# Optimization experiments

Hardware: AMD Instinct MI355X
Metric: run time of the kernel (lower is better)

Reference implementation:

```python
import jax, jax.numpy as jnp
import numpy as np

NEG = -1e30  # finite stand-in for -inf (keeps grads NaN-free)

def _rnnt_costs(log_probs, labels, lengths, label_lengths):
    """RNN-T negative log-likelihood per example.
    log_probs: (N, T, U, V) log-probabilities; labels: (N, U-1) int32;
    lengths, label_lengths: (N,) int32. blank = V-1 (module default).
    alpha recurrence: alpha[t,u] = LSE(alpha[t-1,u]+blank[t-1,u], alpha[t,u-1]+emit[t,u-1]).
    Each row-in-u linear log-recurrence is solved in parallel with cumlogsumexp:
    alpha[t,u] = c[u] + LSE_{k<=u}(A[k] - c[k]),  c = exclusive cumsum of emit[t], A = alpha[t-1]+blank[t-1].
    """
    N, T, U, V = log_probs.shape
    blank = V - 1
    blank_lp = log_probs[..., blank]  # (N, T, U)
    lbl = jnp.broadcast_to(labels[:, None, :, None], (N, T, U - 1, 1))
    emit = jnp.take_along_axis(log_probs[:, :, : U - 1, :], lbl, axis=3)[..., 0]  # (N, T, U-1)

    def row(A, emit_row):
        # A: (N, U) = alpha[t-1] + blank[t-1]; emit_row: (N, U-1) = emit[t]
        c = jnp.concatenate([jnp.zeros((N, 1), log_probs.dtype),
                             jnp.cumsum(emit_row, axis=1)], axis=1)  # (N, U)
        return c + jax.lax.cumlogsumexp(A - c, axis=1)

    A0 = jnp.full((N, U), NEG, log_probs.dtype).at[:, 0].set(0.0)
    alpha0 = row(A0, emit[:, 0, :])  # row t = 0

    def step(alpha_prev, xs):
        blank_prev, emit_row = xs  # (N, U), (N, U-1)
        alpha = row(alpha_prev + blank_prev, emit_row)
        return alpha, alpha

    xs = (jnp.swapaxes(blank_lp[:, :-1, :], 0, 1),  # (T-1, N, U)
          jnp.swapaxes(emit[:, 1:, :], 0, 1))       # (T-1, N, U-1)
    _, alphas = jax.lax.scan(step, alpha0, xs)
    alphas = jnp.concatenate([alpha0[None], alphas], axis=0)  # (T, N, U)

    n = jnp.arange(N)
    t_idx = lengths.astype(jnp.int32) - 1
    u_idx = label_lengths.astype(jnp.int32)
    loglik = alphas[t_idx, n, u_idx] + blank_lp[n, t_idx, u_idx]
    return -loglik  # (N,)


def setup_inputs() -> dict:
    key = jax.random.key(0)
    k1, k2, k3, k4 = jax.random.split(key, 4)
    N, T, U, V = 16, 256, 128, 256
    logits = jax.random.normal(k1, (N, T, U, V), dtype=jnp.float32)
    log_probs = jax.nn.log_softmax(logits, axis=-1)
    labels = jax.random.randint(k2, (N, U - 1), 0, V - 1, dtype=jnp.int32)  # never blank
    lengths = jax.random.randint(k3, (N,), T // 2, T + 1, dtype=jnp.int32).at[0].set(T)
    label_lengths = jax.random.randint(k4, (N,), (U - 1) // 2, U, dtype=jnp.int32).at[0].set(U - 1)
    return {"log_probs": log_probs, "labels": labels,
            "lengths": lengths, "label_lengths": label_lengths}


def reference(log_probs, labels, lengths, label_lengths):
    costs = _rnnt_costs(log_probs, labels, lengths, label_lengths)
    return jnp.mean(costs)  # reduction='mean'
```

## Files before the change

kernel.cpp:

```cpp
#include <hip/hip_runtime.h>


#define T_DIM 256
#define U_DIM 128
#define V_DIM 256
#define UV (U_DIM * V_DIM)
#define GROWS (T_DIM + 1)
#define NEGF (-1e30f)
#define LOG2E 1.44269504088896340736f
#define LN2F  0.69314718055994530942f

__device__ __forceinline__ float lse2b2(float x, float y) {
    float m = fmaxf(x, y);
    float t = __builtin_amdgcn_exp2f(-fabsf(x - y));
    return m + __builtin_amdgcn_logf(1.0f + t);
}

__device__ __forceinline__ float wave_shr1(float x) {
    int xi = __float_as_int(x);
    int r = __builtin_amdgcn_update_dpp(xi, xi, 0x138, 0xF, 0xF, false);
    return __int_as_float(r);
}

__global__ __launch_bounds__(128) void rnnt_gather_kernel(
        const float* __restrict__ lp, const int* __restrict__ labels,
        float2* __restrict__ G) {
    const int t = blockIdx.x;
    const int n = blockIdx.y;
    const int u = threadIdx.x;

    float x = NEGF, y = NEGF;
    if (t >= 1) {
        x = lp[((size_t)(n * T_DIM + (t - 1)) * U_DIM + u) * V_DIM + (V_DIM - 1)]
            * LOG2E;
    }
    if (u >= 1 && t < T_DIM) {
        const int lbl = labels[n * (U_DIM - 1) + (u - 1)];
        y = lp[((size_t)(n * T_DIM + t) * U_DIM + (u - 1)) * V_DIM + lbl] * LOG2E;
    }
    G[(size_t)n * GROWS * U_DIM + t * U_DIM + u] = make_float2(x, y);
}

__global__ __launch_bounds__(64, 1) void rnnt_diag_kernel(
        const float* __restrict__ lp, const float2* __restrict__ G,
        const int* __restrict__ lengths, const int* __restrict__ lab_lens,
        float* __restrict__ out, float inv_n) {
    const int n    = blockIdx.x;
    const int lane = threadIdx.x;
    const int u0   = lane * 2;
    const int u1   = u0 + 1;

    const float2* Gn = G + (size_t)n * GROWS * U_DIM;
    const float2* g0 = Gn + u0;
    const float2* g1 = Gn + u1;

    const int t_len = lengths[n];
    const int u_len = lab_lens[n];
    const int dstar = (t_len - 1) + u_len;

    const float bl = lp[(size_t)n * T_DIM * UV + (size_t)(t_len - 1) * UV
                        + u_len * V_DIM + (V_DIM - 1)];

    float a0 = (lane == 0) ? 0.0f : NEGF;
    float a1 = NEGF;
    float res = NEGF;
    if (dstar == 0 && lane == 0) res = a0;

    float nb = wave_shr1(a1);

    constexpr int PF = 16;
    float2 bufG0[PF], bufG1[PF];

    auto issue = [&](int d, int slot) {
        const int t0 = min(max(d - u0, 0), GROWS - 1);
        const int t1 = min(max(d - u1, 0), GROWS - 1);
        bufG0[slot] = g0[t0 * U_DIM];
        bufG1[slot] = g1[t1 * U_DIM];
    };

#pragma unroll
    for (int j = 0; j < PF; ++j) issue(1 + j, j);

    for (int dd = 1; dd < 385; dd += PF) {
#pragma unroll
        for (int j = 0; j < PF; ++j) {
            const int d = dd + j;
            const int t0 = d - u0;
            const int t1 = d - u1;
            const bool vb0 = (unsigned)(t0 - 1) < (unsigned)(T_DIM - 1);
            const bool vb1 = (unsigned)(t1 - 1) < (unsigned)(T_DIM - 1);
            const bool ve0 = (u0 >= 1) && ((unsigned)t0 < (unsigned)T_DIM);
            const bool ve1 = ((unsigned)t1 < (unsigned)T_DIM);

            const float pa0 = vb0 ? (a0 + bufG0[j].x) : NEGF;
            const float pb0 = ve0 ? (nb + bufG0[j].y) : NEGF;
            const float na0 = lse2b2(pa0, pb0);

            const float pa1 = vb1 ? (a1 + bufG1[j].x) : NEGF;
            const float pb1 = ve1 ? (a0 + bufG1[j].y) : NEGF;
            const float na1 = lse2b2(pa1, pb1);

            a0 = na0;
            a1 = na1;
            nb = wave_shr1(a1);

            issue(d + PF, j);

            if (d == dstar) {
                if (u_len == u0)      res = na0;
                else if (u_len == u1) res = na1;
            }
        }
    }

    if (lane == (u_len >> 1)) {
        atomicAdd(out, -(res * LN2F + bl) * inv_n);
    }
}

extern "C" void kernel_launch(void* const* d_in, const int* in_sizes, int n_in,
                              void* d_out, int out_size, void* d_ws, size_t ws_size,
                              hipStream_t stream) {
    const float* lp      = (const float*)d_in[0];
    const int*   labels  = (const int*)d_in[1];
    const int*   lengths = (const int*)d_in[2];
    const int*   lablens = (const int*)d_in[3];
    float* out = (float*)d_out;
    const int N = in_sizes[2];

    float2* G = (float2*)d_ws;

    hipMemsetAsync(d_out, 0, sizeof(float), stream);
    rnnt_gather_kernel<<<dim3(GROWS, N), dim3(128), 0, stream>>>(lp, labels, G);
    rnnt_diag_kernel<<<dim3(N), dim3(64), 0, stream>>>(
        lp, G, lengths, lablens, out, 1.0f / (float)N);
}
```

Before: 657.5 us.

## Relayout gathered blank/emit values into anti-diagonal order for coalesced loads

```diff
diff --git a/kernel.cpp b/kernel.cpp
--- a/kernel.cpp
+++ b/kernel.cpp
@@ -6,6 +6,7 @@
 #define V_DIM 256
 #define UV (U_DIM * V_DIM)
 #define GROWS (T_DIM + 1)
+#define E_ROWS 384
 #define NEGF (-1e30f)
 #define LOG2E 1.44269504088896340736f
 #define LN2F  0.69314718055994530942f
@@ -41,8 +42,20 @@
     G[(size_t)n * GROWS * U_DIM + t * U_DIM + u] = make_float2(x, y);
 }
 
+__global__ __launch_bounds__(128) void rnnt_relayout_kernel(
+        const float2* __restrict__ G, float2* __restrict__ Gd) {
+    const int e = blockIdx.x;
+    const int n = blockIdx.y;
+    const int u = threadIdx.x;
+    const int t = e - u;
+    float2 v = make_float2(NEGF, NEGF);
+    if ((unsigned)t <= (unsigned)T_DIM)
+        v = G[(size_t)n * GROWS * U_DIM + t * U_DIM + u];
+    Gd[(size_t)n * E_ROWS * U_DIM + e * U_DIM + u] = v;
+}
+
 __global__ __launch_bounds__(64, 1) void rnnt_diag_kernel(
-        const float* __restrict__ lp, const float2* __restrict__ G,
+        const float* __restrict__ lp, const float2* __restrict__ Gd,
         const int* __restrict__ lengths, const int* __restrict__ lab_lens,
         float* __restrict__ out, float inv_n) {
     const int n    = blockIdx.x;
@@ -50,9 +63,7 @@
     const int u0   = lane * 2;
     const int u1   = u0 + 1;
 
-    const float2* Gn = G + (size_t)n * GROWS * U_DIM;
-    const float2* g0 = Gn + u0;
-    const float2* g1 = Gn + u1;
+    const float4* Gdn = (const float4*)(Gd + (size_t)n * E_ROWS * U_DIM);
 
     const int t_len = lengths[n];
     const int u_len = lab_lens[n];
@@ -69,13 +80,11 @@
     float nb = wave_shr1(a1);
 
     constexpr int PF = 16;
-    float2 bufG0[PF], bufG1[PF];
+    float4 buf[PF];
 
     auto issue = [&](int d, int slot) {
-        const int t0 = min(max(d - u0, 0), GROWS - 1);
-        const int t1 = min(max(d - u1, 0), GROWS - 1);
-        bufG0[slot] = g0[t0 * U_DIM];
-        bufG1[slot] = g1[t1 * U_DIM];
+        const int e = min(d, E_ROWS - 1);
+        buf[slot] = Gdn[(size_t)e * 64 + lane];
     };
 
 #pragma unroll
@@ -92,12 +101,12 @@
             const bool ve0 = (u0 >= 1) && ((unsigned)t0 < (unsigned)T_DIM);
             const bool ve1 = ((unsigned)t1 < (unsigned)T_DIM);
 
-            const float pa0 = vb0 ? (a0 + bufG0[j].x) : NEGF;
-            const float pb0 = ve0 ? (nb + bufG0[j].y) : NEGF;
+            const float pa0 = vb0 ? (a0 + buf[j].x) : NEGF;
+            const float pb0 = ve0 ? (nb + buf[j].y) : NEGF;
             const float na0 = lse2b2(pa0, pb0);
 
-            const float pa1 = vb1 ? (a1 + bufG1[j].x) : NEGF;
-            const float pb1 = ve1 ? (a0 + bufG1[j].y) : NEGF;
+            const float pa1 = vb1 ? (a1 + buf[j].z) : NEGF;
+            const float pb1 = ve1 ? (a0 + buf[j].w) : NEGF;
             const float na1 = lse2b2(pa1, pb1);
 
             a0 = na0;
@@ -128,10 +137,12 @@
     float* out = (float*)d_out;
     const int N = in_sizes[2];
 
-    float2* G = (float2*)d_ws;
+    float2* G  = (float2*)d_ws;
+    float2* Gd = G + (size_t)N * GROWS * U_DIM;
 
     hipMemsetAsync(d_out, 0, sizeof(float), stream);
     rnnt_gather_kernel<<<dim3(GROWS, N), dim3(128), 0, stream>>>(lp, labels, G);
+    rnnt_relayout_kernel<<<dim3(E_ROWS, N), dim3(128), 0, stream>>>(G, Gd);
     rnnt_diag_kernel<<<dim3(N), dim3(64), 0, stream>>>(
-        lp, G, lengths, lablens, out, 1.0f / (float)N);
+        lp, Gd, lengths, lablens, out, 1.0f / (float)N);
 }
```

Result: no change. 645.9 us (-1.8%).
